# Kernel tuning notes

Hardware: AMD Instinct MI355X
Metric: run time of the kernel (lower is better)

Reference implementation:

```python
import jax, jax.numpy as jnp
import numpy as np

EMBED_DIM = 1024
NUM_HEADS = 16
HEAD_DIM = EMBED_DIM // NUM_HEADS
ROPE_THETA = 10000.0


def setup_inputs() -> dict:
    key = jax.random.key(0)
    k1, k2, k3, k4, k5 = jax.random.split(key, 5)
    B, S, E = 2, 2048, EMBED_DIM
    scale = 1.0 / np.sqrt(E)
    x = jax.random.normal(k1, (B, S, E), dtype=jnp.float32)
    w_qkv = jax.random.normal(k2, (E, 3 * E), dtype=jnp.float32) * scale
    b_qkv = jnp.zeros((3 * E,), dtype=jnp.float32)
    w_o = jax.random.normal(k3, (E, E), dtype=jnp.float32) * scale
    b_o = jnp.zeros((E,), dtype=jnp.float32)
    return {"x": x, "w_qkv": w_qkv, "b_qkv": b_qkv, "w_o": w_o, "b_o": b_o}


def _rope_cos_sin(seq_len, dtype):
    # half-dim frequencies, GPT-NeoX rotate-half convention
    inv_freq = 1.0 / (ROPE_THETA ** (jnp.arange(0, HEAD_DIM, 2, dtype=jnp.float32) / HEAD_DIM))
    pos = jnp.arange(seq_len, dtype=jnp.float32)
    freqs = pos[:, None] * inv_freq[None, :]          # [S, hd/2]
    emb = jnp.concatenate([freqs, freqs], axis=-1)    # [S, hd]
    return jnp.cos(emb).astype(dtype), jnp.sin(emb).astype(dtype)


def _rotate_half(t):
    t1, t2 = jnp.split(t, 2, axis=-1)
    return jnp.concatenate([-t2, t1], axis=-1)


def reference(x, w_qkv, b_qkv, w_o, b_o):
    B, S, E = x.shape
    H, D = NUM_HEADS, HEAD_DIM
    qkv = x @ w_qkv + b_qkv                            # [B, S, 3E]
    q, k, v = jnp.split(qkv, 3, axis=-1)
    # [B, H, S, D]
    q = q.reshape(B, S, H, D).transpose(0, 2, 1, 3)
    k = k.reshape(B, S, H, D).transpose(0, 2, 1, 3)
    v = v.reshape(B, S, H, D).transpose(0, 2, 1, 3)
    cos, sin = _rope_cos_sin(S, x.dtype)               # [S, D]
    q = q * cos + _rotate_half(q) * sin
    k = k * cos + _rotate_half(k) * sin
    scores = jnp.einsum('bhqd,bhkd->bhqk', q, k) / jnp.sqrt(jnp.asarray(D, x.dtype))
    causal = jnp.tril(jnp.ones((S, S), dtype=bool))
    scores = jnp.where(causal, scores, jnp.asarray(-1e30, x.dtype))
    attn = jax.nn.softmax(scores, axis=-1)
    out = jnp.einsum('bhqk,bhkd->bhqd', attn, v)       # [B, H, S, D]
    out = out.transpose(0, 2, 1, 3).reshape(B, S, E)
    return out @ w_o + b_o
```

## Files before the change

### kernel.cpp

```cpp
#include <hip/hip_runtime.h>
#include <hip/hip_bf16.h>

typedef __hip_bfloat16 bf16_t;
typedef __attribute__((ext_vector_type(8))) __bf16 bf16x8;
typedef __attribute__((ext_vector_type(4))) float f32x4;
typedef __attribute__((ext_vector_type(4))) unsigned short ushort4v;
typedef __attribute__((ext_vector_type(4))) short short4v;

#define NUM_B 2
#define NUM_H 16
#define SEQ   2048
#define EMB   1024
#define LOG2E 1.44269504088896340736f
#define LN10K 13.287712379549449f

__global__ __launch_bounds__(256) void prep_kernel(
    const float* __restrict__ x, const float* __restrict__ wq,
    const float* __restrict__ wo, bf16_t* __restrict__ xb,
    bf16_t* __restrict__ wqT, bf16_t* __restrict__ woT) {
  __shared__ float tile[32][33];
  int bid = blockIdx.x, tid = threadIdx.x;
  if (bid < 4096) {
    int i = (bid * 256 + tid) * 4;
    f32x4 v = *(const f32x4*)&x[i];
    ushort4v p;
#pragma unroll
    for (int j = 0; j < 4; ++j)
      p[j] = __builtin_bit_cast(unsigned short, __float2bfloat16(v[j]));
    *(ushort4v*)&xb[i] = p;
    return;
  }
  const float* src;
  bf16_t* dst;
  int R, C, c0, r0;
  if (bid < 4096 + 3072) {
    int b = bid - 4096;
    src = wq; dst = wqT; R = 1024; C = 3072;
    c0 = (b % 96) * 32; r0 = (b / 96) * 32;
  } else {
    int b = bid - 7168;
    src = wo; dst = woT; R = 1024; C = 1024;
    c0 = (b % 32) * 32; r0 = (b / 32) * 32;
  }
  int tx = tid & 31, ty = tid >> 5;
#pragma unroll
  for (int i = 0; i < 4; ++i)
    tile[ty + i * 8][tx] = src[(size_t)(r0 + ty + i * 8) * C + c0 + tx];
  __syncthreads();
#pragma unroll
  for (int i = 0; i < 4; ++i)
    dst[(size_t)(c0 + ty + i * 8) * R + r0 + tx] = __float2bfloat16(tile[tx][ty + i * 8]);
}

template <int CH>
__device__ __forceinline__ void stage_tile(const bf16_t* __restrict__ G,
                                           int row0, int col0, int ld,
                                           bf16_t* Ls, int tid) {
#pragma unroll
  for (int r = 0; r < CH; ++r) {
    int c = tid + r * 256;
    int row = c >> 2, g = c & 3;
    const char* gp = (const char*)(G + (size_t)(row0 + row) * ld + col0) +
                     ((g ^ ((row >> 1) & 3)) * 16);
    char* lp = (char*)Ls + c * 16;
    __builtin_amdgcn_global_load_lds((const __attribute__((address_space(1))) void*)gp,
                                     (__attribute__((address_space(3))) void*)lp, 16, 0, 0);
  }
}

template <int MODE, int MT>
__global__ __launch_bounds__(256) void gemm_bf16_kernel(
    const bf16_t* __restrict__ A, const bf16_t* __restrict__ Bt,
    const float* __restrict__ bias, bf16_t* __restrict__ out0,
    bf16_t* __restrict__ out1, bf16_t* __restrict__ out2,
    float* __restrict__ outf, int Ndim, int Kdim) {
  __shared__ __align__(16) bf16_t As[MT * 32 * 32];
  __shared__ __align__(16) bf16_t Bs[128 * 32];
  int tid = threadIdx.x;
  int wave = tid >> 6, lane = tid & 63;
  int lr = lane & 15, lq = lane >> 4;
  int m0 = blockIdx.x * (32 * MT), n0 = blockIdx.y * 128;
  int wm = (wave >> 1) * (MT * 16), wn = (wave & 1) * 64;
  int key = (lr >> 1) & 3;
  int goff = ((lq ^ key) * 8);
  f32x4 acc[MT][4];
#pragma unroll
  for (int i = 0; i < MT; ++i)
#pragma unroll
    for (int j = 0; j < 4; ++j) acc[i][j] = (f32x4){0.f, 0.f, 0.f, 0.f};

  for (int k0 = 0; k0 < Kdim; k0 += 32) {
    __syncthreads();
    stage_tile<MT / 2>(A, m0, k0, Kdim, As, tid);
    stage_tile<2>(Bt, n0, k0, Kdim, Bs, tid);
    __syncthreads();
    bf16x8 af[MT], bfr[4];
#pragma unroll
    for (int mt = 0; mt < MT; ++mt)
      af[mt] = *(const bf16x8*)&As[(wm + mt * 16 + lr) * 32 + goff];
#pragma unroll
    for (int nt = 0; nt < 4; ++nt)
      bfr[nt] = *(const bf16x8*)&Bs[(wn + nt * 16 + lr) * 32 + goff];
#pragma unroll
    for (int mt = 0; mt < MT; ++mt)
#pragma unroll
      for (int nt = 0; nt < 4; ++nt)
        acc[mt][nt] = __builtin_amdgcn_mfma_f32_16x16x32_bf16(af[mt], bfr[nt], acc[mt][nt], 0, 0, 0);
  }

  if (MODE == 0) {
#pragma unroll
    for (int pr = 0; pr < 2; ++pr) {
      int na = n0 + wn + pr * 16 + lr;
      int nb = na + 32;
      int sec = na >> 10;
      int h = (na >> 6) & (NUM_H - 1);
      int da = na & 63;
      float bva = bias[na], bvb = bias[nb];
      if (sec == 2) {
#pragma unroll
        for (int mt = 0; mt < MT; ++mt) {
          int mbase = m0 + wm + mt * 16 + lq * 4;
          int b = mbase >> 11;
          int s = mbase & (SEQ - 1);
          int bh = b * NUM_H + h;
          ushort4v pa, pb;
#pragma unroll
          for (int r = 0; r < 4; ++r) {
            pa[r] = __builtin_bit_cast(unsigned short, __float2bfloat16(acc[mt][pr][r] + bva));
            pb[r] = __builtin_bit_cast(unsigned short, __float2bfloat16(acc[mt][pr + 2][r] + bvb));
          }
          *(ushort4v*)&out2[((size_t)bh * 64 + da) * SEQ + s] = pa;
          *(ushort4v*)&out2[((size_t)bh * 64 + da + 32) * SEQ + s] = pb;
        }
      } else {
        bf16_t* dst = (sec == 0) ? out0 : out1;
        float scale = (sec == 0) ? 0.125f : 1.0f;
        int i = da & 31;
        float inv = exp2f(-(float)i * (LN10K / 32.0f));
#pragma unroll
        for (int mt = 0; mt < MT; ++mt) {
          int mbase = m0 + wm + mt * 16 + lq * 4;
          int b = mbase >> 11;
          int s0 = mbase & (SEQ - 1);
          int bh = b * NUM_H + h;
#pragma unroll
          for (int r = 0; r < 4; ++r) {
            float sn, cs;
            sincosf((float)(s0 + r) * inv, &sn, &cs);
            float va = acc[mt][pr][r] + bva;
            float vb = acc[mt][pr + 2][r] + bvb;
            float oa = (va * cs - vb * sn) * scale;
            float ob = (vb * cs + va * sn) * scale;
            size_t rowb = ((size_t)bh * SEQ + (s0 + r)) * 64;
            dst[rowb + da] = __float2bfloat16(oa);
            dst[rowb + da + 32] = __float2bfloat16(ob);
          }
        }
      }
    }
  } else {
#pragma unroll
    for (int nt = 0; nt < 4; ++nt) {
      int n = n0 + wn + nt * 16 + lr;
      float bv = bias[n];
#pragma unroll
      for (int mt = 0; mt < MT; ++mt)
#pragma unroll
        for (int r = 0; r < 4; ++r) {
          int m = m0 + wm + mt * 16 + lq * 4 + r;
          outf[(size_t)m * Ndim + n] = acc[mt][nt][r] + bv;
        }
    }
  }
}

__device__ __forceinline__ void stage_sw(const char* __restrict__ gbase,
                                         size_t rowStride, bf16_t* lds, int tid) {
#pragma unroll
  for (int r = 0; r < 2; ++r) {
    int c = tid + r * 256;
    int row = c >> 3, g = c & 7;
    const char* gp = gbase + (size_t)row * rowStride + ((g ^ (row & 7)) * 16);
    char* lp = (char*)lds + c * 16;
    __builtin_amdgcn_global_load_lds((const __attribute__((address_space(1))) void*)gp,
                                     (__attribute__((address_space(3))) void*)lp, 16, 0, 0);
  }
}

__global__ __launch_bounds__(256) void flash_attn_kernel(
    const bf16_t* __restrict__ Q, const bf16_t* __restrict__ K,
    const bf16_t* __restrict__ Vt, bf16_t* __restrict__ O) {
  __shared__ __align__(16) bf16_t Ks[2][64 * 64];
  __shared__ __align__(16) bf16_t Vs[2][64 * 64];
  int tid = threadIdx.x;
  int wv = tid >> 6, lane = tid & 63;
  int lr = lane & 15, lq = lane >> 4;
  int bx = blockIdx.x;
  int bh = bx & 31;
  int tile = 31 - (bx >> 5);
  int qw0 = tile * 64 + wv * 16;
  const bf16_t* Qb = Q + (size_t)bh * SEQ * 64;
  const bf16_t* Kb = K + (size_t)bh * SEQ * 64;
  const bf16_t* Vb = Vt + (size_t)bh * 64 * SEQ;
  int sw = lr & 7;
  int g0 = (lq ^ sw) * 8;
  int g1 = g0 ^ 32;

  bf16x8 aq0 = *(const bf16x8*)&Qb[(size_t)(qw0 + lr) * 64 + lq * 8];
  bf16x8 aq1 = *(const bf16x8*)&Qb[(size_t)(qw0 + lr) * 64 + 32 + lq * 8];

  f32x4 Oacc[4];
#pragma unroll
  for (int dt = 0; dt < 4; ++dt) Oacc[dt] = (f32x4){0.f, 0.f, 0.f, 0.f};
  float lrow = 0.f;

  int nch = tile + 1;
  stage_sw((const char*)Kb, 128, Ks[0], tid);
  stage_sw((const char*)Vb, SEQ * 2, Vs[0], tid);

  for (int ch = 0; ch < nch; ++ch) {
    int cur = ch & 1;
    bool diag = (ch == tile);
    __syncthreads();
    if (ch + 1 < nch) {
      int kvn = (ch + 1) * 64;
      stage_sw((const char*)(Kb + (size_t)kvn * 64), 128, Ks[cur ^ 1], tid);
      stage_sw((const char*)Vb + (size_t)kvn * 2, SEQ * 2, Vs[cur ^ 1], tid);
    }

#pragma unroll
    for (int sub = 0; sub < 4; ++sub) {
      if (!diag || sub <= wv) {
        int rk = (sub * 16 + lr) * 64;
        bf16x8 k0 = *(const bf16x8*)&Ks[cur][rk + g0];
        bf16x8 k1 = *(const bf16x8*)&Ks[cur][rk + g1];
        f32x4 t = (f32x4){0.f, 0.f, 0.f, 0.f};
        t = __builtin_amdgcn_mfma_f32_16x16x32_bf16(k0, aq0, t, 0, 0, 0);
        t = __builtin_amdgcn_mfma_f32_16x16x32_bf16(k1, aq1, t, 0, 0, 0);
        if (diag && sub == wv) {
#pragma unroll
          for (int r = 0; r < 4; ++r)
            if (lq * 4 + r > lr) t[r] = -1e30f;
        }
        short4v pp;
#pragma unroll
        for (int r = 0; r < 4; ++r) {
          float p = exp2f(t[r] * LOG2E);
          lrow += p;
          pp[r] = __builtin_bit_cast(short, __float2bfloat16(p));
        }
#pragma unroll
        for (int dt = 0; dt < 4; ++dt) {
          int row = dt * 16 + lr;
          int grp = (sub * 2 + (lq >> 1)) ^ sw;
          short4v av = *(const short4v*)&Vs[cur][row * 64 + grp * 8 + (lq & 1) * 4];
          Oacc[dt] = __builtin_amdgcn_mfma_f32_16x16x16bf16_1k(av, pp, Oacc[dt], 0, 0, 0);
        }
      }
    }
  }

  lrow += __shfl_xor(lrow, 16, 64);
  lrow += __shfl_xor(lrow, 32, 64);

  int b = bh >> 4, h = bh & (NUM_H - 1);
  int q = qw0 + lr;
  size_t base = (((size_t)b * SEQ + q) * NUM_H + h) * 64;
  float rinv = 1.0f / lrow;
#pragma unroll
  for (int dt = 0; dt < 4; ++dt) {
    ushort4v ok;
#pragma unroll
    for (int r = 0; r < 4; ++r)
      ok[r] = __builtin_bit_cast(unsigned short, __float2bfloat16(Oacc[dt][r] * rinv));
    *(ushort4v*)&O[base + dt * 16 + lq * 4] = ok;
  }
}

extern "C" void kernel_launch(void* const* d_in, const int* in_sizes, int n_in,
                              void* d_out, int out_size, void* d_ws, size_t ws_size,
                              hipStream_t stream) {
  const float* x      = (const float*)d_in[0];
  const float* w_qkv  = (const float*)d_in[1];
  const float* b_qkv  = (const float*)d_in[2];
  const float* w_o    = (const float*)d_in[3];
  const float* b_o    = (const float*)d_in[4];
  float* out = (float*)d_out;

  bf16_t* ws    = (bf16_t*)d_ws;
  bf16_t* xb    = ws;
  bf16_t* wqkvT = xb + 4 * 1024 * 1024;
  bf16_t* woT   = wqkvT + 3072 * 1024;
  bf16_t* Qb    = woT + 1024 * 1024;
  bf16_t* Kb    = Qb + 4 * 1024 * 1024;
  bf16_t* Vt    = Kb + 4 * 1024 * 1024;
  bf16_t* attn  = Vt + 4 * 1024 * 1024;

  prep_kernel<<<8192, 256, 0, stream>>>(x, w_qkv, w_o, xb, wqkvT, woT);
  gemm_bf16_kernel<0, 4><<<dim3(32, 24), 256, 0, stream>>>(
      xb, wqkvT, b_qkv, Qb, Kb, Vt, nullptr, 3072, 1024);
  flash_attn_kernel<<<1024, 256, 0, stream>>>(Qb, Kb, Vt, attn);
  gemm_bf16_kernel<1, 2><<<dim3(64, 8), 256, 0, stream>>>(
      attn, woT, b_o, nullptr, nullptr, nullptr, out, 1024, 1024);
}
```

Before: 184.6 us.

## Replace QKV GEMM with 256x256-tile 8-wave phased pipelined kernel

Adds a new QKV projection GEMM that uses 256x256 output tiles, 512 threads and 64-deep K slices double-buffered in LDS. The loop is split into four phases, each interleaving LDS fragment loads, async global-to-LDS staging of the next half-tile and an MFMA burst at raised priority. The goal is to hide memory latency and raise MFMA utilization. The fused epilogue (bias, RoPE, Q scaling, V transpose) is reimplemented. The cost is 128KB of LDS, which restricts occupancy, and a grid of only 192 blocks, fewer than the CU count.

```diff
diff --git a/kernel.cpp b/kernel.cpp
--- a/kernel.cpp
+++ b/kernel.cpp
@@ -50,6 +50,204 @@
 #pragma unroll
   for (int i = 0; i < 4; ++i)
     dst[(size_t)(c0 + ty + i * 8) * R + r0 + tx] = __float2bfloat16(tile[tx][ty + i * 8]);
+}
+
+__device__ __forceinline__ void stage_half(const bf16_t* __restrict__ G,
+                                           int row0, int k0, int ld,
+                                           bf16_t* Ls, int tid) {
+#pragma unroll
+  for (int r = 0; r < 2; ++r) {
+    int c = tid + r * 512;
+    int row = c >> 3, g = c & 7;
+    const char* gp = (const char*)(G + (size_t)(row0 + row) * ld + k0) +
+                     ((g ^ (row & 7)) * 16);
+    char* lp = (char*)Ls + c * 16;
+    __builtin_amdgcn_global_load_lds((const __attribute__((address_space(1))) void*)gp,
+                                     (__attribute__((address_space(3))) void*)lp, 16, 0, 0);
+  }
+}
+
+__global__ __launch_bounds__(512, 2) void gemm_qkv_8ph(
+    const bf16_t* __restrict__ A, const bf16_t* __restrict__ Bt,
+    const float* __restrict__ bias, bf16_t* __restrict__ out0,
+    bf16_t* __restrict__ out1, bf16_t* __restrict__ out2) {
+  __shared__ __align__(16) bf16_t As[2][256 * 64];
+  __shared__ __align__(16) bf16_t Bs[2][256 * 64];
+  const int Kd = 1024;
+  const int NT = 16;
+  int tid = threadIdx.x;
+  int wave = tid >> 6, lane = tid & 63;
+  int lr = lane & 15, lq = lane >> 4;
+  int wm = wave >> 2, wn = wave & 3;
+  int m0 = blockIdx.x * 256, n0 = blockIdx.y * 256;
+  int sw = lr & 7;
+  int gk0 = (lq ^ sw) * 16;
+  int gk1 = ((4 + lq) ^ sw) * 16;
+
+  f32x4 acc[8][4];
+#pragma unroll
+  for (int i = 0; i < 8; ++i)
+#pragma unroll
+    for (int j = 0; j < 4; ++j) acc[i][j] = (f32x4){0.f, 0.f, 0.f, 0.f};
+
+  stage_half(A, m0, 0, Kd, &As[0][0], tid);
+  stage_half(A, m0 + 128, 0, Kd, &As[0][128 * 64], tid);
+  stage_half(Bt, n0, 0, Kd, &Bs[0][0], tid);
+  stage_half(Bt, n0 + 128, 0, Kd, &Bs[0][128 * 64], tid);
+  stage_half(A, m0, 64, Kd, &As[1][0], tid);
+  asm volatile("s_waitcnt vmcnt(2)" ::: "memory");
+  __builtin_amdgcn_s_barrier();
+
+  bf16x8 af[4][2], blo[2][2], bhi[2][2];
+  int aw = wm * 128, bw = wn * 64;
+
+#pragma unroll 2
+  for (int t = 0; t < NT; ++t) {
+    int cur = t & 1, nxt = cur ^ 1;
+    const char* Ac = (const char*)As[cur];
+    const char* Bc = (const char*)Bs[cur];
+
+#pragma unroll
+    for (int mi = 0; mi < 4; ++mi) {
+      int ro = (aw + mi * 16 + lr) * 128;
+      af[mi][0] = *(const bf16x8*)(Ac + ro + gk0);
+      af[mi][1] = *(const bf16x8*)(Ac + ro + gk1);
+    }
+#pragma unroll
+    for (int nj = 0; nj < 2; ++nj) {
+      int ro = (bw + nj * 16 + lr) * 128;
+      blo[nj][0] = *(const bf16x8*)(Bc + ro + gk0);
+      blo[nj][1] = *(const bf16x8*)(Bc + ro + gk1);
+    }
+    if (t + 1 < NT) stage_half(A, m0 + 128, (t + 1) * 64, Kd, &As[nxt][128 * 64], tid);
+    __builtin_amdgcn_s_barrier();
+    asm volatile("s_waitcnt lgkmcnt(0)" ::: "memory");
+    __builtin_amdgcn_s_setprio(1);
+#pragma unroll
+    for (int mi = 0; mi < 4; ++mi)
+#pragma unroll
+      for (int nj = 0; nj < 2; ++nj) {
+        acc[mi][nj] = __builtin_amdgcn_mfma_f32_16x16x32_bf16(af[mi][0], blo[nj][0], acc[mi][nj], 0, 0, 0);
+        acc[mi][nj] = __builtin_amdgcn_mfma_f32_16x16x32_bf16(af[mi][1], blo[nj][1], acc[mi][nj], 0, 0, 0);
+      }
+    __builtin_amdgcn_s_setprio(0);
+    __builtin_amdgcn_s_barrier();
+
+#pragma unroll
+    for (int nj = 0; nj < 2; ++nj) {
+      int ro = (bw + (nj + 2) * 16 + lr) * 128;
+      bhi[nj][0] = *(const bf16x8*)(Bc + ro + gk0);
+      bhi[nj][1] = *(const bf16x8*)(Bc + ro + gk1);
+    }
+    if (t + 1 < NT) stage_half(Bt, n0, (t + 1) * 64, Kd, &Bs[nxt][0], tid);
+    __builtin_amdgcn_s_barrier();
+    asm volatile("s_waitcnt lgkmcnt(0)" ::: "memory");
+    __builtin_amdgcn_s_setprio(1);
+#pragma unroll
+    for (int mi = 0; mi < 4; ++mi)
+#pragma unroll
+      for (int nj = 0; nj < 2; ++nj) {
+        acc[mi][nj + 2] = __builtin_amdgcn_mfma_f32_16x16x32_bf16(af[mi][0], bhi[nj][0], acc[mi][nj + 2], 0, 0, 0);
+        acc[mi][nj + 2] = __builtin_amdgcn_mfma_f32_16x16x32_bf16(af[mi][1], bhi[nj][1], acc[mi][nj + 2], 0, 0, 0);
+      }
+    __builtin_amdgcn_s_setprio(0);
+    __builtin_amdgcn_s_barrier();
+
+#pragma unroll
+    for (int mi = 0; mi < 4; ++mi) {
+      int ro = (aw + (mi + 4) * 16 + lr) * 128;
+      af[mi][0] = *(const bf16x8*)(Ac + ro + gk0);
+      af[mi][1] = *(const bf16x8*)(Ac + ro + gk1);
+    }
+    if (t + 1 < NT) stage_half(Bt, n0 + 128, (t + 1) * 64, Kd, &Bs[nxt][128 * 64], tid);
+    __builtin_amdgcn_s_barrier();
+    asm volatile("s_waitcnt lgkmcnt(0)" ::: "memory");
+    __builtin_amdgcn_s_setprio(1);
+#pragma unroll
+    for (int mi = 0; mi < 4; ++mi)
+#pragma unroll
+      for (int nj = 0; nj < 2; ++nj) {
+        acc[mi + 4][nj + 2] = __builtin_amdgcn_mfma_f32_16x16x32_bf16(af[mi][0], bhi[nj][0], acc[mi + 4][nj + 2], 0, 0, 0);
+        acc[mi + 4][nj + 2] = __builtin_amdgcn_mfma_f32_16x16x32_bf16(af[mi][1], bhi[nj][1], acc[mi + 4][nj + 2], 0, 0, 0);
+      }
+    __builtin_amdgcn_s_setprio(0);
+    __builtin_amdgcn_s_barrier();
+
+#pragma unroll
+    for (int nj = 0; nj < 2; ++nj) {
+      int ro = (bw + nj * 16 + lr) * 128;
+      blo[nj][0] = *(const bf16x8*)(Bc + ro + gk0);
+      blo[nj][1] = *(const bf16x8*)(Bc + ro + gk1);
+    }
+    if (t + 2 < NT) stage_half(A, m0, (t + 2) * 64, Kd, &As[cur][0], tid);
+    __builtin_amdgcn_s_barrier();
+    asm volatile("s_waitcnt lgkmcnt(0)" ::: "memory");
+    __builtin_amdgcn_s_setprio(1);
+#pragma unroll
+    for (int mi = 0; mi < 4; ++mi)
+#pragma unroll
+      for (int nj = 0; nj < 2; ++nj) {
+        acc[mi + 4][nj] = __builtin_amdgcn_mfma_f32_16x16x32_bf16(af[mi][0], blo[nj][0], acc[mi + 4][nj], 0, 0, 0);
+        acc[mi + 4][nj] = __builtin_amdgcn_mfma_f32_16x16x32_bf16(af[mi][1], blo[nj][1], acc[mi + 4][nj], 0, 0, 0);
+      }
+    __builtin_amdgcn_s_setprio(0);
+    if (t + 1 < NT) {
+      if (t + 2 < NT) asm volatile("s_waitcnt vmcnt(2)" ::: "memory");
+      else            asm volatile("s_waitcnt vmcnt(0)" ::: "memory");
+      __builtin_amdgcn_s_barrier();
+    }
+  }
+
+#pragma unroll
+  for (int pr = 0; pr < 2; ++pr) {
+    int na = n0 + wn * 64 + pr * 16 + lr;
+    int nb = na + 32;
+    int sec = na >> 10;
+    int h = (na >> 6) & (NUM_H - 1);
+    int da = na & 63;
+    float bva = bias[na], bvb = bias[nb];
+    if (sec == 2) {
+#pragma unroll
+      for (int mi = 0; mi < 8; ++mi) {
+        int mbase = m0 + wm * 128 + mi * 16 + lq * 4;
+        int b = mbase >> 11;
+        int s = mbase & (SEQ - 1);
+        int bh = b * NUM_H + h;
+        ushort4v pa, pb;
+#pragma unroll
+        for (int r = 0; r < 4; ++r) {
+          pa[r] = __builtin_bit_cast(unsigned short, __float2bfloat16(acc[mi][pr][r] + bva));
+          pb[r] = __builtin_bit_cast(unsigned short, __float2bfloat16(acc[mi][pr + 2][r] + bvb));
+        }
+        *(ushort4v*)&out2[((size_t)bh * 64 + da) * SEQ + s] = pa;
+        *(ushort4v*)&out2[((size_t)bh * 64 + da + 32) * SEQ + s] = pb;
+      }
+    } else {
+      bf16_t* dst = (sec == 0) ? out0 : out1;
+      float scale = (sec == 0) ? 0.125f : 1.0f;
+      int i = da & 31;
+      float inv = exp2f(-(float)i * (LN10K / 32.0f));
+#pragma unroll
+      for (int mi = 0; mi < 8; ++mi) {
+        int mbase = m0 + wm * 128 + mi * 16 + lq * 4;
+        int b = mbase >> 11;
+        int s0 = mbase & (SEQ - 1);
+        int bh = b * NUM_H + h;
+#pragma unroll
+        for (int r = 0; r < 4; ++r) {
+          float sn, cs;
+          sincosf((float)(s0 + r) * inv, &sn, &cs);
+          float va = acc[mi][pr][r] + bva;
+          float vb = acc[mi][pr + 2][r] + bvb;
+          float oa = (va * cs - vb * sn) * scale;
+          float ob = (vb * cs + va * sn) * scale;
+          size_t rowb = ((size_t)bh * SEQ + (s0 + r)) * 64;
+          dst[rowb + da] = __float2bfloat16(oa);
+          dst[rowb + da + 32] = __float2bfloat16(ob);
+        }
+      }
+    }
+  }
 }
 
 template <int CH>
@@ -298,8 +496,7 @@
   bf16_t* attn  = Vt + 4 * 1024 * 1024;
 
   prep_kernel<<<8192, 256, 0, stream>>>(x, w_qkv, w_o, xb, wqkvT, woT);
-  gemm_bf16_kernel<0, 4><<<dim3(32, 24), 256, 0, stream>>>(
-      xb, wqkvT, b_qkv, Qb, Kb, Vt, nullptr, 3072, 1024);
+  gemm_qkv_8ph<<<dim3(16, 12), 512, 0, stream>>>(xb, wqkvT, b_qkv, Qb, Kb, Vt);
   flash_attn_kernel<<<1024, 256, 0, stream>>>(Qb, Kb, Vt, attn);
   gemm_bf16_kernel<1, 2><<<dim3(64, 8), 256, 0, stream>>>(
       attn, woT, b_o, nullptr, nullptr, nullptr, out, 1024, 1024);
```

New measurement: 209.7 us. 13.6% more time.
